# Performance work log

Hardware: AMD Instinct MI355X
Metric: run time of the kernel (lower is better)

The kernel has to match this reference:

```python
import jax, jax.numpy as jnp
import numpy as np
from jax import lax

D_MODEL = 512
D_INNER = 1024   # expand=2
D_STATE = 16
D_CONV = 4
DT_RANK = 32     # ceil(d_model/16)
D_FFN = 2048
EPS = 1e-6


def _layernorm(x, g, b):
    mu = jnp.mean(x, axis=-1, keepdims=True)
    var = jnp.mean((x - mu) ** 2, axis=-1, keepdims=True)
    return (x - mu) * lax.rsqrt(var + EPS) * g + b


def _mamba(x, in_w, conv_w, conv_b, xproj_w, dt_w, dt_b, A_log, D_vec, out_w):
    # x: [B, L, d_model]
    B, L, _ = x.shape
    xz = jnp.einsum('bld,ed->ble', x, in_w)           # [B, L, 2*d_inner]
    xc, z = xz[..., :D_INNER], xz[..., D_INNER:]
    # causal depthwise conv over time
    xt = xc.transpose(0, 2, 1)                        # [B, d_inner, L]
    kern = conv_w[:, None, :]                         # [d_inner, 1, d_conv]
    xt = lax.conv_general_dilated(xt, kern, (1,), [(D_CONV - 1, 0)],
                                  feature_group_count=D_INNER)
    xc = jax.nn.silu(xt.transpose(0, 2, 1) + conv_b)  # [B, L, d_inner]
    # input-dependent SSM parameters
    x_dbl = jnp.einsum('bld,ed->ble', xc, xproj_w)    # [B, L, dt_rank+2*d_state]
    dt = x_dbl[..., :DT_RANK]
    Bm = x_dbl[..., DT_RANK:DT_RANK + D_STATE]
    Cm = x_dbl[..., DT_RANK + D_STATE:]
    delta = jax.nn.softplus(jnp.einsum('blr,dr->bld', dt, dt_w) + dt_b)  # [B, L, d_inner]
    A = -jnp.exp(A_log)                               # [d_inner, d_state]

    def step(h, inp):
        d_t, u_t, b_t, c_t = inp                      # [B,di],[B,di],[B,ds],[B,ds]
        dA = jnp.exp(d_t[:, :, None] * A)             # [B, di, ds]
        dBu = (d_t * u_t)[:, :, None] * b_t[:, None, :]
        h = dA * h + dBu
        y = jnp.einsum('bds,bs->bd', h, c_t)
        return h, y

    h0 = jnp.zeros((B, D_INNER, D_STATE), x.dtype)
    xs = (delta.transpose(1, 0, 2), xc.transpose(1, 0, 2),
          Bm.transpose(1, 0, 2), Cm.transpose(1, 0, 2))
    _, ys = lax.scan(step, h0, xs)                    # [L, B, d_inner]
    y = ys.transpose(1, 0, 2) + xc * D_vec
    y = y * jax.nn.silu(z)
    return jnp.einsum('ble,de->bld', y, out_w)        # [B, L, d_model]


def setup_inputs() -> dict:
    key = jax.random.key(0)
    ks = iter(jax.random.split(key, 40))
    B, S, T = 8, 512, 1024

    def nrm(shape, scale=0.02):
        return jax.random.normal(next(ks), shape, dtype=jnp.float32) * scale

    def mamba_params(prefix):
        A_log = jnp.log(jnp.broadcast_to(jnp.arange(1, D_STATE + 1, dtype=jnp.float32),
                                         (D_INNER, D_STATE)))
        return {
            prefix + '_in_w': nrm((2 * D_INNER, D_MODEL)),
            prefix + '_conv_w': nrm((D_INNER, D_CONV), 0.1),
            prefix + '_conv_b': jnp.zeros((D_INNER,), jnp.float32),
            prefix + '_xproj_w': nrm((DT_RANK + 2 * D_STATE, D_INNER)),
            prefix + '_dt_w': nrm((D_INNER, DT_RANK), 0.1),
            prefix + '_dt_b': jnp.full((D_INNER,), -4.0, jnp.float32),
            prefix + '_A_log': A_log,
            prefix + '_D_vec': jnp.ones((D_INNER,), jnp.float32),
            prefix + '_out_w': nrm((D_MODEL, D_INNER)),
        }

    inp = {
        'tgt': jax.random.normal(next(ks), (B, S, D_MODEL), dtype=jnp.float32),
        'memory': jax.random.normal(next(ks), (B, T, D_MODEL), dtype=jnp.float32),
    }
    inp.update(mamba_params('self'))
    inp.update(mamba_params('cross'))
    inp.update({
        'ln1_g': jnp.ones((D_MODEL,), jnp.float32), 'ln1_b': jnp.zeros((D_MODEL,), jnp.float32),
        'ln2_g': jnp.ones((D_MODEL,), jnp.float32), 'ln2_b': jnp.zeros((D_MODEL,), jnp.float32),
        'ln3_g': jnp.ones((D_MODEL,), jnp.float32), 'ln3_b': jnp.zeros((D_MODEL,), jnp.float32),
        'ffn_w1': nrm((D_FFN, D_MODEL)), 'ffn_b1': jnp.zeros((D_FFN,), jnp.float32),
        'ffn_w2': nrm((D_MODEL, D_FFN)), 'ffn_b2': jnp.zeros((D_MODEL,), jnp.float32),
    })
    return inp


def reference(tgt, memory,
              self_in_w, self_conv_w, self_conv_b, self_xproj_w, self_dt_w, self_dt_b,
              self_A_log, self_D_vec, self_out_w,
              cross_in_w, cross_conv_w, cross_conv_b, cross_xproj_w, cross_dt_w, cross_dt_b,
              cross_A_log, cross_D_vec, cross_out_w,
              ln1_g, ln1_b, ln2_g, ln2_b, ln3_g, ln3_b,
              ffn_w1, ffn_b1, ffn_w2, ffn_b2):
    S = tgt.shape[1]
    # self-Mamba block (post-norm, dropout=0)
    t2 = _mamba(tgt, self_in_w, self_conv_w, self_conv_b, self_xproj_w,
                self_dt_w, self_dt_b, self_A_log, self_D_vec, self_out_w)
    t = _layernorm(tgt + t2, ln1_g, ln1_b)
    # cross-Mamba: scan over [memory; tgt], keep last S steps
    cat = jnp.concatenate([memory, t], axis=1)
    c2 = _mamba(cat, cross_in_w, cross_conv_w, cross_conv_b, cross_xproj_w,
                cross_dt_w, cross_dt_b, cross_A_log, cross_D_vec, cross_out_w)[:, -S:]
    t = _layernorm(t + c2, ln2_g, ln2_b)
    # positionwise FFN
    f = jnp.einsum('bld,fd->blf', t, ffn_w1) + ffn_b1
    f = jax.nn.relu(f)
    f = jnp.einsum('blf,df->bld', f, ffn_w2) + ffn_b2
    t = _layernorm(t + f, ln3_g, ln3_b)
    return t
```

## Files before the change

kernel.cpp:

```cpp
#include <hip/hip_runtime.h>
#include <math.h>

#define DM    512
#define DI    1024
#define DSN   16
#define DTR   32
#define DFFN  2048
#define BB    8
#define SS    512
#define TTM   1024
#define LCAT  1536
#define CONV_R 8

#define ACT_NONE     0
#define ACT_RELU     1
#define ACT_DELTA    3
#define ACT_XDBL     4

typedef __attribute__((ext_vector_type(8))) short short8;
typedef __attribute__((ext_vector_type(8))) unsigned short ushort8;
typedef __attribute__((ext_vector_type(4))) float f32x4;

#define L2E 1.4426950408889634f

__device__ __forceinline__ unsigned short f2b(float f) {
    unsigned int u = __float_as_uint(f);
    return (unsigned short)((u + 0x7FFFu + ((u >> 16) & 1u)) >> 16);
}
__device__ __forceinline__ float b2f(unsigned short h) {
    return __uint_as_float(((unsigned int)h) << 16);
}
__device__ __forceinline__ float fast_softplus(float v) {
    return (v > 20.f) ? v : __logf(1.f + __expf(v));
}
__device__ __forceinline__ float fexp2(float x) {
#if __has_builtin(__builtin_amdgcn_exp2f)
    return __builtin_amdgcn_exp2f(x);
#else
    float r; asm("v_exp_f32 %0, %1" : "=v"(r) : "v"(x)); return r;
#endif
}
__device__ __forceinline__ float frcp(float x) {
    return __builtin_amdgcn_rcpf(x);
}
__device__ __forceinline__ void gld16(const void* g, void* l) {
    __builtin_amdgcn_global_load_lds(
        (const __attribute__((address_space(1))) void*)g,
        (__attribute__((address_space(3))) void*)l, 16, 0, 0);
}

__device__ __forceinline__ int map_row(int m, int mb, int bs, int ro) {
    int q = m / mb;
    return q * bs + ro + (m - q * mb);
}

__global__ __launch_bounds__(256) void mgemm_kernel(
    const unsigned short* __restrict__ A, int mb, int bs, int ro,
    const unsigned short* __restrict__ W, const float* __restrict__ bias,
    float* __restrict__ Cf, unsigned short* __restrict__ Cb,
    float* __restrict__ C2, float* __restrict__ Cf2,
    int N, int K, int act,
    int omb, int obs, int oro, int ldc, int nofs, int pstr,
    int ysplit, int amb2, int abs2, int aro2, int wofs2,
    int omb2, int obs2, int oro2, int nofs2)
{
    __shared__ __align__(16) unsigned short As[128 * 64];
    __shared__ __align__(16) unsigned short Bs[128 * 64];
    int tid = threadIdx.x;
    int lane = tid & 63, wave = tid >> 6;
    int wy = wave >> 1, wx = wave & 1;
    int bx = blockIdx.x, by = blockIdx.y;
    int nx = gridDim.x, ny = gridDim.y;
    const unsigned short* Wp = W;
    if (ysplit) {
        if (by >= ysplit) {
            by -= ysplit; ny = gridDim.y - ysplit;
            mb = amb2; bs = abs2; ro = aro2; Wp += wofs2;
            omb = omb2; obs = obs2; oro = oro2; nofs = nofs2;
        } else ny = ysplit;
    }
    int f = by * nx + bx;
    int xcd = f & 7, j2 = f >> 3;
    int bandh = ny >> 3;
    int m0 = (xcd * bandh + j2 / nx) * 128;
    int n0 = (j2 % nx) * 128;
    int Kh = K / gridDim.z;
    int kbeg = blockIdx.z * Kh, kend = kbeg + Kh;
    float* Cfo = Cf;
    const float* biaso = bias;
    if (blockIdx.z) { Cfo = Cf2 + (size_t)(blockIdx.z - 1) * pstr; biaso = nullptr; }

    unsigned aoff[4], boff[4];
    unsigned short* la[4];
    unsigned short* lb[4];
    #pragma unroll
    for (int j = 0; j < 4; j++) {
        int c  = wave * 256 + j * 64 + lane;
        int r  = c >> 3;
        int q  = c & 7;
        int g  = q ^ (r & 7);
        int arow = map_row(m0 + r, mb, bs, ro);
        aoff[j] = (unsigned)(arow * K + g * 8);
        boff[j] = (unsigned)((n0 + r) * K + g * 8);
        la[j] = As + (size_t)(wave * 256 + j * 64) * 8;
        lb[j] = Bs + (size_t)(wave * 256 + j * 64) * 8;
    }
    int fm = lane & 15, fg = lane >> 4;
    int sw = fg ^ (fm & 3);
    int b2 = (fm >> 2) & 1;
    const unsigned short* arp = As + ((size_t)(wy * 64 + fm) * 8 + sw) * 8;
    const unsigned short* brp = Bs + ((size_t)(wx * 64 + fm) * 8 + sw) * 8;

    f32x4 acc[4][4];
    #pragma unroll
    for (int i = 0; i < 4; i++)
        #pragma unroll
        for (int j = 0; j < 4; j++) acc[i][j] = 0.f;

    for (int k0 = kbeg; k0 < kend; k0 += 64) {
        #pragma unroll
        for (int j = 0; j < 4; j++) {
            gld16(A  + aoff[j] + k0, la[j]);
            gld16(Wp + boff[j] + k0, lb[j]);
        }
        __syncthreads();
        #pragma unroll
        for (int h = 0; h < 2; h++) {
            int ho = ((h ^ b2) * 32);
            short8 af[4], bfr[4];
            #pragma unroll
            for (int t = 0; t < 4; t++) af[t]  = *(const short8*)(arp + ho + t * 1024);
            #pragma unroll
            for (int t = 0; t < 4; t++) bfr[t] = *(const short8*)(brp + ho + t * 1024);
            #pragma unroll
            for (int i = 0; i < 4; i++)
                #pragma unroll
                for (int j = 0; j < 4; j++)
                    acc[i][j] = __builtin_amdgcn_mfma_f32_16x16x32_bf16(af[i], bfr[j], acc[i][j], 0, 0, 0);
        }
        __syncthreads();
    }

    int en = lane & 15, em = (lane >> 4) * 4;
    if (act == ACT_XDBL) {
        size_t zb = (size_t)blockIdx.z * omb;
        #pragma unroll
        for (int j = 0; j < 4; j++) {
            int n = n0 + wx * 64 + j * 16 + en;
            if (n >= 64) continue;
            #pragma unroll
            for (int i = 0; i < 4; i++) {
                int mbase = m0 + wy * 64 + i * 16 + em;
                #pragma unroll
                for (int r = 0; r < 4; r++)
                    C2[(zb + mbase + r) * 64 + n] = acc[i][j][r];
            }
        }
        return;
    }
    if (act == ACT_DELTA) {
        #pragma unroll
        for (int j = 0; j < 4; j++) {
            int n = n0 + wx * 64 + j * 16 + en;
            float bv = bias[n];
            #pragma unroll
            for (int i = 0; i < 4; i++) {
                int mbase = m0 + wy * 64 + i * 16 + em;
                #pragma unroll
                for (int r = 0; r < 4; r++) {
                    float v = acc[i][j][r] + bv;
                    Cb[(size_t)(mbase + r) * 1024 + n] = f2b(fast_softplus(v));
                }
            }
        }
        return;
    }
    #pragma unroll
    for (int j = 0; j < 4; j++) {
        int n = n0 + wx * 64 + j * 16 + en;
        float bv = biaso ? biaso[n] : 0.f;
        #pragma unroll
        for (int i = 0; i < 4; i++) {
            int mbase = m0 + wy * 64 + i * 16 + em;
            #pragma unroll
            for (int r = 0; r < 4; r++) {
                float v = acc[i][j][r] + bv;
                if (act == ACT_RELU) v = v > 0.f ? v : 0.f;
                int orow = map_row(mbase + r, omb, obs, oro);
                size_t off = (size_t)orow * ldc + nofs + n;
                if (Cb) Cb[off] = f2b(v);
                else    Cfo[off] = v;
            }
        }
    }
}

__global__ __launch_bounds__(256) void xdbl_combine(
    const float* __restrict__ pxd, unsigned short* __restrict__ dtb,
    float* __restrict__ bcout, int M, int Z)
{
    int idx = blockIdx.x * 256 + threadIdx.x;
    int m = idx >> 4, n4 = idx & 15;
    int n = n4 * 4;
    float4 s = make_float4(0.f, 0.f, 0.f, 0.f);
    for (int z = 0; z < Z; z++) {
        float4 p = *(const float4*)(pxd + ((size_t)z * M + m) * 64 + n);
        s.x += p.x; s.y += p.y; s.z += p.z; s.w += p.w;
    }
    if (n < 32) {
        ((ushort4*)(dtb + (size_t)m * 64))[n4] =
            make_ushort4(f2b(s.x), f2b(s.y), f2b(s.z), f2b(s.w));
    } else {
        *(float4*)(bcout + (size_t)m * 32 + (n - 32)) = s;
        ((ushort4*)(dtb + (size_t)m * 64))[n4] = make_ushort4(0, 0, 0, 0);
    }
}

struct PrepPtrs {
    const float* tgt; const float* mem;
    const float* w[6];
    const float* xpj_s; const float* xpj_c;
    const float* dtw_s; const float* dtw_c;
    unsigned short* tgtb; unsigned short* catb; unsigned short* wb;
    unsigned short* xprojb_s; unsigned short* xprojb_c;
    unsigned short* dtwb_s; unsigned short* dtwb_c;
};
__global__ __launch_bounds__(256) void prep_kernel(PrepPtrs p)
{
    int u = blockIdx.x * 256 + threadIdx.x;
    if (u < 524288) {
        float4 v = ((const float4*)p.tgt)[u];
        ((ushort4*)p.tgtb)[u] = make_ushort4(f2b(v.x), f2b(v.y), f2b(v.z), f2b(v.w));
        return;
    }
    if (u < 1572864) {
        int f = u - 524288;
        int b = f >> 17, rem = f & 131071;
        float4 v = ((const float4*)p.mem)[f];
        ((ushort4*)p.catb)[(size_t)b * 196608 + rem] =
            make_ushort4(f2b(v.x), f2b(v.y), f2b(v.z), f2b(v.w));
        return;
    }
    if (u < 2883584) {
        const int cum[7] = {0, 262144, 524288, 655360, 786432, 1048576, 1310720};
        int i = u - 1572864;
        int seg = 0;
        #pragma unroll
        for (int s = 1; s < 6; s++) seg += (i >= cum[s]);
        float4 v = ((const float4*)p.w[seg])[i - cum[seg]];
        ((ushort4*)p.wb)[i] = make_ushort4(f2b(v.x), f2b(v.y), f2b(v.z), f2b(v.w));
        return;
    }
    if (u < 2949120) {
        int i = u - 2883584;
        const float* src = p.xpj_s;
        unsigned short* dst = p.xprojb_s;
        if (i >= 32768) { i -= 32768; src = p.xpj_c; dst = p.xprojb_c; }
        int n = i >> 8;
        ushort4 o = make_ushort4(0, 0, 0, 0);
        if (n < 64) {
            float4 v = ((const float4*)src)[i];
            o = make_ushort4(f2b(v.x), f2b(v.y), f2b(v.z), f2b(v.w));
        }
        ((ushort4*)dst)[i] = o;
        return;
    }
    {
        int i = u - 2949120;
        const float* src = p.dtw_s;
        unsigned short* dst = p.dtwb_s;
        if (i >= 16384) { i -= 16384; src = p.dtw_c; dst = p.dtwb_c; }
        int n = i >> 4, c = (i & 15) * 4;
        ushort4 o = make_ushort4(0, 0, 0, 0);
        if (c < 32) {
            float4 v = *(const float4*)(src + n * 32 + c);
            o = make_ushort4(f2b(v.x), f2b(v.y), f2b(v.z), f2b(v.w));
        }
        ((ushort4*)dst)[i] = o;
    }
}

__global__ __launch_bounds__(256) void conv_silu_kernel(
    const unsigned short* __restrict__ xz,
    const float* __restrict__ cw,
    const float* __restrict__ cb,
    unsigned short* __restrict__ xc, int L, int total)
{
    int idx = blockIdx.x * blockDim.x + threadIdx.x;
    if (idx >= total) return;
    int d8 = idx & 127;
    int d0 = d8 * 8;
    int t  = idx >> 7;
    int nq = L / CONV_R;
    int b  = t / nq;
    int l0 = (t - b * nq) * CONV_R;
    size_t rbase = (size_t)b * L + l0;

    float4 wv[8];
    #pragma unroll
    for (int j = 0; j < 8; j++) wv[j] = *(const float4*)(cw + (d0 + j) * 4);
    float bias[8];
    {
        float4 c0 = ((const float4*)(cb + d0))[0];
        float4 c1 = ((const float4*)(cb + d0))[1];
        bias[0]=c0.x; bias[1]=c0.y; bias[2]=c0.z; bias[3]=c0.w;
        bias[4]=c1.x; bias[5]=c1.y; bias[6]=c1.z; bias[7]=c1.w;
    }
    ushort8 win[CONV_R + 3];
    #pragma unroll
    for (int k = 0; k < 3; k++) {
        ushort8 z;
        #pragma unroll
        for (int j = 0; j < 8; j++) z[j] = 0;
        win[k] = (l0 - 3 + k >= 0)
            ? *(const ushort8*)(xz + (rbase - 3 + k) * 2048 + d0) : z;
    }
    #pragma unroll
    for (int i = 0; i < CONV_R; i++)
        win[3 + i] = *(const ushort8*)(xz + (rbase + i) * 2048 + d0);

    const float* w = (const float*)&wv[0];
    #pragma unroll
    for (int i = 0; i < CONV_R; i++) {
        float acc[8];
        #pragma unroll
        for (int j = 0; j < 8; j++) acc[j] = bias[j];
        #pragma unroll
        for (int k = 0; k < 4; k++) {
            ushort8 v = win[i + k];
            #pragma unroll
            for (int j = 0; j < 8; j++)
                acc[j] = fmaf(b2f(v[j]), w[j * 4 + k], acc[j]);
        }
        ushort8 o;
        #pragma unroll
        for (int j = 0; j < 8; j++)
            o[j] = f2b(acc[j] * frcp(1.f + __expf(-acc[j])));
        *(ushort8*)(xc + (rbase + i) * 1024 + d0) = o;
    }
}

template<int CH>
__global__ __launch_bounds__(256) void scan_part1(
    const unsigned short* __restrict__ delta, const unsigned short* __restrict__ xc,
    const float* __restrict__ bc, const float* __restrict__ A_log,
    float* __restrict__ part_h, float* __restrict__ part_s, int L, int NCr)
{
    __shared__ float bcs[CH * 16];
    int tid = threadIdx.x;
    int dblk = blockIdx.x & 3;
    int rest = blockIdx.x >> 2;
    int c    = rest % NCr;
    int b    = rest / NCr;
    if (c == NCr - 1) return;
    int l0 = c * CH;
    for (int i = tid; i < CH * 16; i += 256) {
        int lr = i >> 4, s = i & 15;
        bcs[i] = bc[((size_t)b * L + l0 + lr) * 32 + s];
    }
    __syncthreads();
    int d    = dblk * 256 + tid;
    float A2[DSN];
    {
        const float4* ap = (const float4*)(A_log + d * DSN);
        #pragma unroll
        for (int q = 0; q < 4; q++) {
            float4 a4 = ap[q];
            A2[q*4+0] = -__expf(a4.x) * L2E;
            A2[q*4+1] = -__expf(a4.y) * L2E;
            A2[q*4+2] = -__expf(a4.z) * L2E;
            A2[q*4+3] = -__expf(a4.w) * L2E;
        }
    }
    float h[DSN];
    #pragma unroll
    for (int s = 0; s < DSN; s++) h[s] = 0.f;
    float ssum = 0.f;
    size_t rb = (size_t)b * L + l0;
    constexpr int HH = CH / 2;
    #pragma unroll
    for (int hh = 0; hh < 2; hh++) {
        unsigned short dls[HH], uss[HH];
        #pragma unroll
        for (int i = 0; i < HH; i++) {
            size_t rn = rb + hh * HH + i;
            dls[i] = delta[rn * DI + d];
            uss[i] = xc[rn * DI + d];
        }
        #pragma unroll
        for (int i = 0; i < HH; i++) {
            int st = hh * HH + i;
            float cdl = b2f(dls[i]), cu = b2f(uss[i]);
            const float* Bm = bcs + st * 16;
            float du = cdl * cu;
            ssum += cdl;
            #pragma unroll
            for (int s = 0; s < DSN; s++)
                h[s] = fmaf(fexp2(cdl * A2[s]), h[s], du * Bm[s]);
        }
    }
    size_t base = ((size_t)(b * NCr + c) * DSN) * DI + d;
    #pragma unroll
    for (int s = 0; s < DSN; s++)
        part_h[base + (size_t)s * DI] = h[s];
    part_s[(size_t)(b * NCr + c) * DI + d] = ssum;
}

__global__ __launch_bounds__(256) void scan_combine(
    const float* __restrict__ A_log,
    float* __restrict__ part_h, const float* __restrict__ part_s, int NCr, int cwrite)
{
    int idx = blockIdx.x * 256 + threadIdx.x;
    int d  = idx & (DI - 1);
    int s  = (idx >> 10) & (DSN - 1);
    int b  = idx >> 14;
    float A2 = -__expf(A_log[d * DSN + s]) * L2E;
    float h = 0.f;
    size_t sbase = (size_t)b * NCr * DI + d;
    size_t hbase = ((size_t)b * NCr * DSN + s) * DI + d;
    for (int c = 0; c < NCr; c++) {
        float ph = part_h[hbase];
        float S  = part_s[sbase];
        if (c >= cwrite) part_h[hbase] = h;
        h = fmaf(fexp2(A2 * S), h, ph);
        hbase += (size_t)DSN * DI;
        sbase += DI;
    }
}

template<int CH>
__global__ __launch_bounds__(256) void scan_part2(
    const unsigned short* __restrict__ delta, const unsigned short* __restrict__ xc,
    const float* __restrict__ bc, const unsigned short* __restrict__ xz,
    const float* __restrict__ A_log, const float* __restrict__ Dv,
    const float* __restrict__ part_h,
    unsigned short* __restrict__ out, int L, int NCr, int c0, int lmin)
{
    __shared__ float bcs[CH * 32];
    int tid = threadIdx.x;
    int dblk = blockIdx.x & 3;
    int rest = blockIdx.x >> 2;
    int ncp  = NCr - c0;
    int c    = c0 + rest % ncp;
    int b    = rest / ncp;
    int l0 = c * CH;
    for (int i = tid; i < CH * 32; i += 256)
        bcs[i] = bc[((size_t)b * L + l0) * 32 + i];
    __syncthreads();
    int d    = dblk * 256 + tid;
    float A2[DSN];
    {
        const float4* ap = (const float4*)(A_log + d * DSN);
        #pragma unroll
        for (int q = 0; q < 4; q++) {
            float4 a4 = ap[q];
            A2[q*4+0] = -__expf(a4.x) * L2E;
            A2[q*4+1] = -__expf(a4.y) * L2E;
            A2[q*4+2] = -__expf(a4.z) * L2E;
            A2[q*4+3] = -__expf(a4.w) * L2E;
        }
    }
    float Dvd = Dv[d];
    size_t hb = ((size_t)(b * NCr + c) * DSN) * DI + d;
    float h[DSN];
    #pragma unroll
    for (int s = 0; s < DSN; s++) h[s] = part_h[hb + (size_t)s * DI];
    size_t rb = (size_t)b * L + l0;
    constexpr int HH = CH / 2;
    #pragma unroll
    for (int hh = 0; hh < 2; hh++) {
        unsigned short dls[HH], uss[HH], zs[HH];
        #pragma unroll
        for (int i = 0; i < HH; i++) {
            size_t rn = rb + hh * HH + i;
            dls[i] = delta[rn * DI + d];
            uss[i] = xc[rn * DI + d];
            zs[i]  = xz[rn * 2048 + DI + d];
        }
        #pragma unroll
        for (int i = 0; i < HH; i++) {
            int st = hh * HH + i;
            float cdl = b2f(dls[i]), cu = b2f(uss[i]);
            const float* Bm = bcs + st * 32;
            const float* Cm = Bm + DSN;
            float du = cdl * cu;
            float y = 0.f;
            #pragma unroll
            for (int s = 0; s < DSN; s++) {
                h[s] = fmaf(fexp2(cdl * A2[s]), h[s], du * Bm[s]);
                y = fmaf(h[s], Cm[s], y);
            }
            if (l0 + st >= lmin) {
                float cz = b2f(zs[i]);
                float sil = cz * frcp(1.f + __expf(-cz));
                out[(rb + st) * DI + d] = f2b((y + cu * Dvd) * sil);
            }
        }
    }
}

__global__ __launch_bounds__(128) void addln_kernel(
    const float* __restrict__ a, int amb, int absd, int aro, int lda,
    const float* __restrict__ bsrc, const float* __restrict__ parts, int nparts, int pstr,
    const float* __restrict__ g, const float* __restrict__ be,
    float* __restrict__ outf, int omb, int obsd, int oro, int ldo,
    unsigned short* __restrict__ outb, int bmb, int bbsd, int bro, int ldb)
{
    int m = blockIdx.x, t = threadIdx.x;
    int ar = map_row(m, amb, absd, aro);
    float4 x4 = ((const float4*)(a + (size_t)ar * lda))[t];
    float4 y4 = ((const float4*)(bsrc + (size_t)m * DM))[t];
    float v[4] = {x4.x + y4.x, x4.y + y4.y, x4.z + y4.z, x4.w + y4.w};
    for (int p = 0; p < nparts; p++) {
        float4 z4 = ((const float4*)(parts + (size_t)p * pstr + (size_t)m * DM))[t];
        v[0] += z4.x; v[1] += z4.y; v[2] += z4.z; v[3] += z4.w;
    }
    float sum = v[0] + v[1] + v[2] + v[3];
    float sq  = v[0]*v[0] + v[1]*v[1] + v[2]*v[2] + v[3]*v[3];
    #pragma unroll
    for (int o = 32; o > 0; o >>= 1) {
        sum += __shfl_down(sum, o);
        sq  += __shfl_down(sq, o);
    }
    __shared__ float s0[2], s1[2];
    if ((t & 63) == 0) { s0[t >> 6] = sum; s1[t >> 6] = sq; }
    __syncthreads();
    float tot = s0[0] + s0[1];
    float tsq = s1[0] + s1[1];
    float mu = tot * (1.f / DM);
    float var = tsq * (1.f / DM) - mu * mu;
    float rs = rsqrtf(var + 1e-6f);
    float4 g4 = ((const float4*)g)[t];
    float4 b4 = ((const float4*)be)[t];
    float o0 = (v[0] - mu) * rs * g4.x + b4.x;
    float o1 = (v[1] - mu) * rs * g4.y + b4.y;
    float o2 = (v[2] - mu) * rs * g4.z + b4.z;
    float o3 = (v[3] - mu) * rs * g4.w + b4.w;
    if (outf) {
        int orow = map_row(m, omb, obsd, oro);
        ((float4*)(outf + (size_t)orow * ldo))[t] = make_float4(o0, o1, o2, o3);
    }
    if (outb) {
        int brow = map_row(m, bmb, bbsd, bro);
        ((ushort4*)(outb + (size_t)brow * ldb))[t] =
            make_ushort4(f2b(o0), f2b(o1), f2b(o2), f2b(o3));
    }
}

static void run_scan(const unsigned short* dltb, const unsigned short* xcb, const float* bc,
                     const unsigned short* xzb, const float* A_log, const float* Dv,
                     float* part_h, float* part_s, unsigned short* out, int L, int NCr,
                     int c0, int lmin, hipStream_t stream)
{
    int blocks1 = BB * NCr * (DI / 256);
    int blocks2 = BB * (NCr - c0) * (DI / 256);
    if (L == SS) {
        scan_part1<8><<<blocks1, 256, 0, stream>>>(dltb, xcb, bc, A_log, part_h, part_s, L, NCr);
        scan_combine<<<BB * DI * DSN / 256, 256, 0, stream>>>(A_log, part_h, part_s, NCr, c0);
        scan_part2<8><<<blocks2, 256, 0, stream>>>(dltb, xcb, bc, xzb, A_log, Dv, part_h, out, L, NCr, c0, lmin);
    } else {
        scan_part1<24><<<blocks1, 256, 0, stream>>>(dltb, xcb, bc, A_log, part_h, part_s, L, NCr);
        scan_combine<<<BB * DI * DSN / 256, 256, 0, stream>>>(A_log, part_h, part_s, NCr, c0);
        scan_part2<24><<<blocks2, 256, 0, stream>>>(dltb, xcb, bc, xzb, A_log, Dv, part_h, out, L, NCr, c0, lmin);
    }
}

extern "C" void kernel_launch(void* const* d_in, const int* in_sizes, int n_in,
                              void* d_out, int out_size, void* d_ws, size_t ws_size,
                              hipStream_t stream)
{
    const float* tgt       = (const float*)d_in[0];
    const float* memory    = (const float*)d_in[1];
    const float* s_in_w    = (const float*)d_in[2];
    const float* s_conv_w  = (const float*)d_in[3];
    const float* s_conv_b  = (const float*)d_in[4];
    const float* s_xproj_w = (const float*)d_in[5];
    const float* s_dt_w    = (const float*)d_in[6];
    const float* s_dt_b    = (const float*)d_in[7];
    const float* s_A_log   = (const float*)d_in[8];
    const float* s_D_vec   = (const float*)d_in[9];
    const float* s_out_w   = (const float*)d_in[10];
    const float* c_in_w    = (const float*)d_in[11];
    const float* c_conv_w  = (const float*)d_in[12];
    const float* c_conv_b  = (const float*)d_in[13];
    const float* c_xproj_w = (const float*)d_in[14];
    const float* c_dt_w    = (const float*)d_in[15];
    const float* c_dt_b    = (const float*)d_in[16];
    const float* c_A_log   = (const float*)d_in[17];
    const float* c_D_vec   = (const float*)d_in[18];
    const float* c_out_w   = (const float*)d_in[19];
    const float* ln1_g     = (const float*)d_in[20];
    const float* ln1_b     = (const float*)d_in[21];
    const float* ln2_g     = (const float*)d_in[22];
    const float* ln2_b     = (const float*)d_in[23];
    const float* ln3_g     = (const float*)d_in[24];
    const float* ln3_b     = (const float*)d_in[25];
    const float* ffn_w1    = (const float*)d_in[26];
    const float* ffn_b1    = (const float*)d_in[27];
    const float* ffn_w2    = (const float*)d_in[28];
    const float* ffn_b2    = (const float*)d_in[29];
    float* outp = (float*)d_out;

    float* ws     = (float*)d_ws;
    float* bc     = ws;
    float* t1     = bc     + 393216;
    float* tbuf   = t1     + 2097152;
    float* part_h = tbuf   + 2097152;
    float* proj   = part_h;
    float* pparts = part_h + 2097152;
    float* pxd    = part_h;
    float* part_s = part_h + 8388608;
    unsigned short* ub      = (unsigned short*)(part_s + 524288);
    unsigned short* dltb    = ub;
    unsigned short* catb    = dltb    + 12582912;
    unsigned short* tgtb    = catb    + 6291456;
    unsigned short* xzb     = tgtb    + 2097152;
    unsigned short* xcb     = xzb     + 25165824;
    unsigned short* ygb     = xcb     + 12582912;
    unsigned short* tbbf    = ygb     + 12582912;
    unsigned short* s_in_wb = tbbf    + 2097152;
    unsigned short* c_in_wb = s_in_wb + 1048576;
    unsigned short* s_out_wb= c_in_wb + 1048576;
    unsigned short* c_out_wb= s_out_wb+ 524288;
    unsigned short* w1b     = c_out_wb+ 524288;
    unsigned short* w2b     = w1b     + 1048576;
    unsigned short* xprojb_s= w2b     + 1048576;
    unsigned short* xprojb_c= xprojb_s+ 131072;
    unsigned short* dtwb_s  = xprojb_c+ 131072;
    unsigned short* dtwb_c  = dtwb_s  + 65536;
    unsigned short* dtb     = dtwb_c  + 65536;
    unsigned short* fbuf    = xzb;
    float* ffnout  = (float*)dltb;
    float* fparts  = ffnout + 2097152;

    {
        PrepPtrs pp;
        pp.tgt = tgt; pp.mem = memory;
        pp.w[0]=s_in_w; pp.w[1]=c_in_w; pp.w[2]=s_out_w; pp.w[3]=c_out_w; pp.w[4]=ffn_w1; pp.w[5]=ffn_w2;
        pp.xpj_s = s_xproj_w; pp.xpj_c = c_xproj_w;
        pp.dtw_s = s_dt_w;    pp.dtw_c = c_dt_w;
        pp.tgtb = tgtb; pp.catb = catb; pp.wb = s_in_wb;
        pp.xprojb_s = xprojb_s; pp.xprojb_c = xprojb_c;
        pp.dtwb_s = dtwb_s; pp.dtwb_c = dtwb_c;
        prep_kernel<<<11648, 256, 0, stream>>>(pp);
    }

    mgemm_kernel<<<dim3(2048/128, 4096/128), 256, 0, stream>>>(
        tgtb, 4096, 0, 0, s_in_wb, nullptr, nullptr, xzb, nullptr, nullptr, 2048, 512, ACT_NONE,
        4096, 0, 0, 2048, 0, 0,  0, 0,0,0, 0, 0,0,0, 0);
    conv_silu_kernel<<<(BB*(SS/CONV_R)*128 + 255)/256, 256, 0, stream>>>(
        xzb, s_conv_w, s_conv_b, xcb, SS, BB*(SS/CONV_R)*128);
    mgemm_kernel<<<dim3(1, 4096/128, 4), 256, 0, stream>>>(
        xcb, 4096, 0, 0, xprojb_s, nullptr, nullptr, nullptr, pxd, nullptr, 128, 1024, ACT_XDBL,
        4096, 0, 0, 0, 0, 0,  0, 0,0,0, 0, 0,0,0, 0);
    xdbl_combine<<<4096*16/256, 256, 0, stream>>>(pxd, dtb, bc, 4096, 4);
    mgemm_kernel<<<dim3(1024/128, 4096/128), 256, 0, stream>>>(
        dtb, 4096, 0, 0, dtwb_s, s_dt_b, nullptr, dltb, nullptr, nullptr, 1024, 64, ACT_DELTA,
        4096, 0, 0, 1024, 0, 0,  0, 0,0,0, 0, 0,0,0, 0);
    run_scan(dltb, xcb, bc, xzb, s_A_log, s_D_vec, part_h, part_s, ygb, SS, 64, 0, 0, stream);
    mgemm_kernel<<<dim3(512/128, 4096/128, 4), 256, 0, stream>>>(
        ygb, 4096, 0, 0, s_out_wb, nullptr, proj, nullptr, nullptr, pparts, 512, 1024, ACT_NONE,
        4096, 0, 0, 512, 0, 2097152,  0, 0,0,0, 0, 0,0,0, 0);
    addln_kernel<<<4096, 128, 0, stream>>>(
        tgt, 4096, 0, 0, DM, proj, pparts, 3, 2097152, ln1_g, ln1_b,
        t1, 4096, 0, 0, DM, catb, 512, 1536, 1024, DM);

    mgemm_kernel<<<dim3(1024/128, 96 + 32), 256, 0, stream>>>(
        catb, 12288, 0, 0, c_in_wb, nullptr, nullptr, xzb, nullptr, nullptr, 2048, 512, ACT_NONE,
        12288, 0, 0, 2048, 0, 0,
        96, 512, 1536, 1024, 1024 * 512, 512, 1536, 1024, 1024);
    conv_silu_kernel<<<(BB*(LCAT/CONV_R)*128 + 255)/256, 256, 0, stream>>>(
        xzb, c_conv_w, c_conv_b, xcb, LCAT, BB*(LCAT/CONV_R)*128);
    mgemm_kernel<<<dim3(1, 12288/128, 4), 256, 0, stream>>>(
        xcb, 12288, 0, 0, xprojb_c, nullptr, nullptr, nullptr, pxd, nullptr, 128, 1024, ACT_XDBL,
        12288, 0, 0, 0, 0, 0,  0, 0,0,0, 0, 0,0,0, 0);
    xdbl_combine<<<12288*16/256, 256, 0, stream>>>(pxd, dtb, bc, 12288, 4);
    mgemm_kernel<<<dim3(1024/128, 12288/128), 256, 0, stream>>>(
        dtb, 12288, 0, 0, dtwb_c, c_dt_b, nullptr, dltb, nullptr, nullptr, 1024, 64, ACT_DELTA,
        12288, 0, 0, 1024, 0, 0,  0, 0,0,0, 0, 0,0,0, 0);
    run_scan(dltb, xcb, bc, xzb, c_A_log, c_D_vec, part_h, part_s, ygb, LCAT, 64, 42, 1024, stream);
    mgemm_kernel<<<dim3(512/128, 4096/128, 4), 256, 0, stream>>>(
        ygb, 512, 1536, 1024, c_out_wb, nullptr, proj, nullptr, nullptr, pparts, 512, 1024, ACT_NONE,
        4096, 0, 0, 512, 0, 2097152,  0, 0,0,0, 0, 0,0,0, 0);
    addln_kernel<<<4096, 128, 0, stream>>>(
        t1, 4096, 0, 0, DM, proj, pparts, 3, 2097152, ln2_g, ln2_b,
        tbuf, 4096, 0, 0, DM, tbbf, 4096, 0, 0, DM);

    mgemm_kernel<<<dim3(2048/128, 4096/128), 256, 0, stream>>>(
        tbbf, 4096, 0, 0, w1b, ffn_b1, nullptr, fbuf, nullptr, nullptr, 2048, 512, ACT_RELU,
        4096, 0, 0, 2048, 0, 0,  0, 0,0,0, 0, 0,0,0, 0);
    mgemm_kernel<<<dim3(512/128, 4096/128, 4), 256, 0, stream>>>(
        fbuf, 4096, 0, 0, w2b, ffn_b2, ffnout, nullptr, nullptr, fparts, 512, 2048, ACT_NONE,
        4096, 0, 0, 512, 0, 2097152,  0, 0,0,0, 0, 0,0,0, 0);
    addln_kernel<<<4096, 128, 0, stream>>>(
        tbuf, 4096, 0, 0, DM, ffnout, fparts, 3, 2097152, ln3_g, ln3_b,
        outp, 4096, 0, 0, DM, nullptr, 0, 0, 0, 0);
}
```

Before: 491.4 us.

## Add double-buffered 512-thread GEMM with async global-to-LDS loads for bf16-output GEMMs

Adds a new GEMM kernel, mgemm_pipe, using 8 waves per 128x128 tile, a two-stage LDS double buffer filled by direct global-to-LDS loads, swizzled LDS addressing and explicit waitcnt/barrier scheduling. The next K tile is prefetched while MFMAs run on the current one, to hide global memory latency. An XCD-aware block remapping is also included to improve L2 locality. It replaces the original kernel for the three bf16-output GEMMs (self in-proj, cross in-proj, FFN1). In exchange it uses more threads and LDS per block, and correctness depends on the hand-tuned vmcnt counts.

```diff
diff --git a/kernel.cpp b/kernel.cpp
--- a/kernel.cpp
+++ b/kernel.cpp
@@ -190,6 +190,119 @@
                 size_t off = (size_t)orow * ldc + nofs + n;
                 if (Cb) Cb[off] = f2b(v);
                 else    Cfo[off] = v;
+            }
+        }
+    }
+}
+
+__global__ __launch_bounds__(512, 4) void mgemm_pipe(
+    const unsigned short* __restrict__ A, int mb, int bs, int ro,
+    const unsigned short* __restrict__ W, const float* __restrict__ bias,
+    unsigned short* __restrict__ Cb, int K, int act,
+    int omb, int obs, int oro, int ldc, int nofs,
+    int ysplit, int amb2, int abs2, int aro2, int wofs2,
+    int omb2, int obs2, int oro2, int nofs2)
+{
+    __shared__ __align__(16) unsigned short smem[32768];
+    int tid = threadIdx.x;
+    int lane = tid & 63, wave = tid >> 6;
+    int wy = wave >> 2, wx = wave & 3;
+    int bx = blockIdx.x, by = blockIdx.y;
+    int nx = gridDim.x, ny = gridDim.y;
+    const unsigned short* Wp = W;
+    if (ysplit) {
+        if (by >= ysplit) {
+            by -= ysplit; ny = gridDim.y - ysplit;
+            mb = amb2; bs = abs2; ro = aro2; Wp += wofs2;
+            omb = omb2; obs = obs2; oro = oro2; nofs = nofs2;
+        } else ny = ysplit;
+    }
+    int f = by * nx + bx;
+    int xcd = f & 7, j2 = f >> 3;
+    int bandh = ny >> 3;
+    int m0 = (xcd * bandh + j2 / nx) * 128;
+    int n0 = (j2 % nx) * 128;
+
+    int c0 = tid, c1 = tid + 512;
+    int r0 = c0 >> 3, g0 = (c0 & 7) ^ (r0 & 7);
+    int r1 = c1 >> 3, g1 = (c1 & 7) ^ (r1 & 7);
+    unsigned ga0 = (unsigned)(map_row(m0 + r0, mb, bs, ro) * K + g0 * 8);
+    unsigned ga1 = (unsigned)(map_row(m0 + r1, mb, bs, ro) * K + g1 * 8);
+    unsigned gb0 = (unsigned)((n0 + r0) * K + g0 * 8);
+    unsigned gb1 = (unsigned)((n0 + r1) * K + g1 * 8);
+    int uA0 = wave * 512, uA1 = wave * 512 + 4096;
+    int uB0 = 8192 + wave * 512, uB1 = 8192 + 4096 + wave * 512;
+
+#define PSTAGE(kk, bofs) do { \
+    gld16(A  + ga0 + (kk), smem + (bofs) + uA0); \
+    gld16(Wp + gb0 + (kk), smem + (bofs) + uB0); \
+    gld16(A  + ga1 + (kk), smem + (bofs) + uA1); \
+    gld16(Wp + gb1 + (kk), smem + (bofs) + uB1); \
+} while (0)
+
+    int fm = lane & 15, fg = lane >> 4;
+    int sw = fg ^ (fm & 3);
+    int b2 = (fm >> 2) & 1;
+    int arpO = (wy * 64 + fm) * 64 + sw * 8;
+    int brpO = 8192 + (wx * 32 + fm) * 64 + sw * 8;
+
+    f32x4 acc[4][2];
+    #pragma unroll
+    for (int i = 0; i < 4; i++)
+        #pragma unroll
+        for (int j = 0; j < 2; j++) acc[i][j] = 0.f;
+
+    int nk = K >> 6;
+    PSTAGE(0, 0);
+    PSTAGE(64, 16384);
+
+    for (int t = 0; t < nk; ++t) {
+        if (t + 1 < nk) { asm volatile("s_waitcnt vmcnt(4)" ::: "memory"); }
+        else            { asm volatile("s_waitcnt vmcnt(0)" ::: "memory"); }
+        __builtin_amdgcn_s_barrier();
+        __builtin_amdgcn_sched_barrier(0);
+        int bo = (t & 1) << 14;
+        short8 af[2][4], bfr[2][2];
+        #pragma unroll
+        for (int h = 0; h < 2; h++) {
+            int ho = ((h ^ b2) << 5);
+            #pragma unroll
+            for (int i = 0; i < 4; i++)
+                af[h][i] = *(const short8*)(smem + bo + arpO + ho + i * 1024);
+            #pragma unroll
+            for (int j = 0; j < 2; j++)
+                bfr[h][j] = *(const short8*)(smem + bo + brpO + ho + j * 1024);
+        }
+        asm volatile("s_waitcnt lgkmcnt(0)" ::: "memory");
+        __builtin_amdgcn_sched_barrier(0);
+        __builtin_amdgcn_s_barrier();
+        __builtin_amdgcn_sched_barrier(0);
+        if (t + 2 < nk) PSTAGE((t + 2) * 64, bo);
+        #pragma unroll
+        for (int h = 0; h < 2; h++)
+            #pragma unroll
+            for (int i = 0; i < 4; i++)
+                #pragma unroll
+                for (int j = 0; j < 2; j++)
+                    acc[i][j] = __builtin_amdgcn_mfma_f32_16x16x32_bf16(
+                        af[h][i], bfr[h][j], acc[i][j], 0, 0, 0);
+    }
+#undef PSTAGE
+
+    int en = lane & 15, em = (lane >> 4) * 4;
+    #pragma unroll
+    for (int j = 0; j < 2; j++) {
+        int n = n0 + wx * 32 + j * 16 + en;
+        float bv = bias ? bias[n] : 0.f;
+        #pragma unroll
+        for (int i = 0; i < 4; i++) {
+            int mbase = m0 + wy * 64 + i * 16 + em;
+            #pragma unroll
+            for (int r = 0; r < 4; r++) {
+                float v = acc[i][j][r] + bv;
+                if (act == ACT_RELU) v = v > 0.f ? v : 0.f;
+                int orow = map_row(mbase + r, omb, obs, oro);
+                Cb[(size_t)orow * ldc + nofs + n] = f2b(v);
             }
         }
     }
@@ -645,9 +758,9 @@
         prep_kernel<<<11648, 256, 0, stream>>>(pp);
     }
 
-    mgemm_kernel<<<dim3(2048/128, 4096/128), 256, 0, stream>>>(
-        tgtb, 4096, 0, 0, s_in_wb, nullptr, nullptr, xzb, nullptr, nullptr, 2048, 512, ACT_NONE,
-        4096, 0, 0, 2048, 0, 0,  0, 0,0,0, 0, 0,0,0, 0);
+    mgemm_pipe<<<dim3(2048/128, 4096/128), 512, 0, stream>>>(
+        tgtb, 4096, 0, 0, s_in_wb, nullptr, xzb, 512, ACT_NONE,
+        4096, 0, 0, 2048, 0,  0, 0,0,0, 0, 0,0,0, 0);
     conv_silu_kernel<<<(BB*(SS/CONV_R)*128 + 255)/256, 256, 0, stream>>>(
         xzb, s_conv_w, s_conv_b, xcb, SS, BB*(SS/CONV_R)*128);
     mgemm_kernel<<<dim3(1, 4096/128, 4), 256, 0, stream>>>(
@@ -665,9 +778,9 @@
         tgt, 4096, 0, 0, DM, proj, pparts, 3, 2097152, ln1_g, ln1_b,
         t1, 4096, 0, 0, DM, catb, 512, 1536, 1024, DM);
 
-    mgemm_kernel<<<dim3(1024/128, 96 + 32), 256, 0, stream>>>(
-        catb, 12288, 0, 0, c_in_wb, nullptr, nullptr, xzb, nullptr, nullptr, 2048, 512, ACT_NONE,
-        12288, 0, 0, 2048, 0, 0,
+    mgemm_pipe<<<dim3(1024/128, 96 + 32), 512, 0, stream>>>(
+        catb, 12288, 0, 0, c_in_wb, nullptr, xzb, 512, ACT_NONE,
+        12288, 0, 0, 2048, 0,
         96, 512, 1536, 1024, 1024 * 512, 512, 1536, 1024, 1024);
     conv_silu_kernel<<<(BB*(LCAT/CONV_R)*128 + 255)/256, 256, 0, stream>>>(
         xzb, c_conv_w, c_conv_b, xcb, LCAT, BB*(LCAT/CONV_R)*128);
@@ -686,9 +799,9 @@
         t1, 4096, 0, 0, DM, proj, pparts, 3, 2097152, ln2_g, ln2_b,
         tbuf, 4096, 0, 0, DM, tbbf, 4096, 0, 0, DM);
 
-    mgemm_kernel<<<dim3(2048/128, 4096/128), 256, 0, stream>>>(
-        tbbf, 4096, 0, 0, w1b, ffn_b1, nullptr, fbuf, nullptr, nullptr, 2048, 512, ACT_RELU,
-        4096, 0, 0, 2048, 0, 0,  0, 0,0,0, 0, 0,0,0, 0);
+    mgemm_pipe<<<dim3(2048/128, 4096/128), 512, 0, stream>>>(
+        tbbf, 4096, 0, 0, w1b, ffn_b1, fbuf, 512, ACT_RELU,
+        4096, 0, 0, 2048, 0,  0, 0,0,0, 0, 0,0,0, 0);
     mgemm_kernel<<<dim3(512/128, 4096/128, 4), 256, 0, stream>>>(
         fbuf, 4096, 0, 0, w2b, ffn_b2, ffnout, nullptr, nullptr, fparts, 512, 2048, ACT_NONE,
         4096, 0, 0, 512, 0, 2097152,  0, 0,0,0, 0, 0,0,0, 0);
```

Result: no change. 494.7 us (+0.7%).
